# Optimization experiments

Measured on AMD Instinct MI355X. Metric: run time of the kernel, lower is better.

The kernel has to match this reference:

```python
import jax, jax.numpy as jnp
import numpy as np

B, Din, T, G = 8, 512, 1024, 128
DM, H, L, FF = 512, 8, 2, 2048
MAX_PERIOD = 10000.0


def _ln(x, s, b, eps=1e-5):
    m = x.mean(-1, keepdims=True)
    v = ((x - m) ** 2).mean(-1, keepdims=True)
    return (x - m) * jax.lax.rsqrt(v + eps) * s + b


def _rope(x, pos):
    # x: (B,H,S,Dh), pos: (S,)
    dh = x.shape[-1]
    half = dh // 2
    freqs = 1.0 / (MAX_PERIOD ** (jnp.arange(half, dtype=jnp.float32) / half))
    ang = pos[:, None] * freqs[None, :]              # (S, half)
    cos, sin = jnp.cos(ang), jnp.sin(ang)
    x1, x2 = x[..., :half], x[..., half:]
    return jnp.concatenate([x1 * cos - x2 * sin, x1 * sin + x2 * cos], axis=-1)


def _transformer(x, W_in, b_in, ln1_s, ln1_b, Wq, Wk, Wv, Wo, ls1,
                 ln2_s, ln2_b, W1, b1, W2, b2, ls2, lnf_s, lnf_b, W_out, b_out):
    # x: (B, Din, S) conv layout -> (B, S, DM)
    h = jnp.einsum('bds,de->bse', x, W_in) + b_in
    Bx, S, E = h.shape
    dh = E // H
    pos = jnp.arange(S, dtype=jnp.float32)
    scale = 1.0 / jnp.sqrt(jnp.asarray(dh, h.dtype))
    for l in range(Wq.shape[0]):
        y = _ln(h, ln1_s[l], ln1_b[l])
        q = (y @ Wq[l]).reshape(Bx, S, H, dh).transpose(0, 2, 1, 3)
        k = (y @ Wk[l]).reshape(Bx, S, H, dh).transpose(0, 2, 1, 3)
        v = (y @ Wv[l]).reshape(Bx, S, H, dh).transpose(0, 2, 1, 3)
        q, k = _rope(q, pos), _rope(k, pos)
        att = jax.nn.softmax(jnp.einsum('bhqd,bhkd->bhqk', q, k) * scale, axis=-1)
        o = jnp.einsum('bhqk,bhkd->bhqd', att, v).transpose(0, 2, 1, 3).reshape(Bx, S, E)
        h = h + ls1[l] * (o @ Wo[l])
        y = _ln(h, ln2_s[l], ln2_b[l])
        h = h + ls2[l] * (jax.nn.gelu(y @ W1[l] + b1[l]) @ W2[l] + b2[l])
    h = _ln(h, lnf_s, lnf_b)
    return (h @ W_out + b_out).transpose(0, 2, 1)  # (B, Din, S)


def _forward(features, alignment_matrix, num_segments_per_item, params):
    Bx, D, Tt = features.shape
    Gx = alignment_matrix.shape[1]
    ar_t = jnp.arange(Tt, dtype=jnp.int32)
    ar_g = jnp.arange(Gx, dtype=jnp.int32)
    group_mask = ar_g[None, :] < num_segments_per_item[:, None]          # (B,G)
    group_last = (alignment_matrix * ar_t.astype(features.dtype)).max(axis=2).astype(jnp.int32)  # (B,G)
    valid_last = jnp.where(group_mask, group_last, -1)
    frame_lengths = valid_last.max(axis=1) + 1                            # (B,)
    frame_mask = ar_t[None, :] < frame_lengths[:, None]                   # (B,T)
    last_for_count = jnp.where(group_mask, group_last, Tt + 1)
    num_q_before = jnp.sum(last_for_count[:, :, None] < ar_t[None, None, :], axis=1).astype(jnp.int32)  # (B,T)
    frame_dest = ar_t[None, :] + num_q_before                             # (B,T)
    query_dest = group_last + ar_g[None, :] + 1                           # (B,G)
    # mean-pooled query init
    summed = jnp.einsum('bgt,bdt->bgd', alignment_matrix, features)
    counts = jnp.maximum(alignment_matrix.sum(axis=2), 1.0)
    queries = (summed / counts[..., None]).transpose(0, 2, 1)             # (B,D,G)
    source_seq = jnp.concatenate([features, queries], axis=2)             # (B,D,T+G)
    dest = jnp.concatenate([frame_dest, query_dest], axis=1)              # (B,T+G)
    smask = jnp.concatenate([frame_mask, group_mask], axis=1)
    dest_m = jnp.where(smask, dest, Tt + Gx)
    perm = jnp.argsort(dest_m, axis=1)                                    # (B,T+G)
    interleaved = jnp.take_along_axis(source_seq, perm[:, None, :], axis=2)
    tout = _transformer(interleaved, *params)                             # (B,D,T+G)
    inv_perm = jnp.argsort(perm, axis=1)
    qpos = inv_perm[:, Tt:]                                               # (B,G)
    agg = jnp.take_along_axis(tout, qpos[:, None, :], axis=2)             # (B,D,G)
    return jnp.where(group_mask[:, None, :], agg, 0.0)


def setup_inputs() -> dict:
    key = jax.random.key(0)
    ks = jax.random.split(key, 8)
    rng = np.random.default_rng(0)
    align = np.zeros((B, G, T), np.float32)
    num_seg = np.zeros((B,), np.int32)
    for b in range(B):
        n = int(rng.integers(G // 2, G + 1))
        cuts = np.sort(rng.choice(np.arange(1, T), n - 1, replace=False))
        gid = np.searchsorted(cuts, np.arange(T), side='right')
        align[b, gid, np.arange(T)] = 1.0
        num_seg[b] = n
    s = 0.02
    return {
        'features': jax.random.normal(ks[0], (B, Din, T), jnp.float32),
        'alignment_matrix': jnp.asarray(align),
        'num_segments_per_item': jnp.asarray(num_seg),
        'W_in': jax.random.normal(ks[1], (Din, DM), jnp.float32) * s,
        'b_in': jnp.zeros((DM,), jnp.float32),
        'ln1_s': jnp.ones((L, DM), jnp.float32), 'ln1_b': jnp.zeros((L, DM), jnp.float32),
        'Wq': jax.random.normal(ks[2], (L, DM, DM), jnp.float32) * s,
        'Wk': jax.random.normal(ks[3], (L, DM, DM), jnp.float32) * s,
        'Wv': jax.random.normal(ks[4], (L, DM, DM), jnp.float32) * s,
        'Wo': jax.random.normal(ks[5], (L, DM, DM), jnp.float32) * s,
        'ls1': 0.01 * jnp.ones((L, DM), jnp.float32),
        'ln2_s': jnp.ones((L, DM), jnp.float32), 'ln2_b': jnp.zeros((L, DM), jnp.float32),
        'W1': jax.random.normal(ks[6], (L, DM, FF), jnp.float32) * s,
        'b1': jnp.zeros((L, FF), jnp.float32),
        'W2': jax.random.normal(ks[7], (L, FF, DM), jnp.float32) * s,
        'b2': jnp.zeros((L, DM), jnp.float32),
        'ls2': 0.01 * jnp.ones((L, DM), jnp.float32),
        'lnf_s': jnp.ones((DM,), jnp.float32), 'lnf_b': jnp.zeros((DM,), jnp.float32),
        'W_out': jax.random.normal(jax.random.fold_in(key, 9), (DM, Din), jnp.float32) * s,
        'b_out': jnp.zeros((Din,), jnp.float32),
    }


def reference(features, alignment_matrix, num_segments_per_item, W_in, b_in, ln1_s, ln1_b,
              Wq, Wk, Wv, Wo, ls1, ln2_s, ln2_b, W1, b1, W2, b2, ls2, lnf_s, lnf_b, W_out, b_out):
    params = (W_in, b_in, ln1_s, ln1_b, Wq, Wk, Wv, Wo, ls1,
              ln2_s, ln2_b, W1, b1, W2, b2, ls2, lnf_s, lnf_b, W_out, b_out)
    return _forward(features, alignment_matrix, num_segments_per_item, params)
```

## Files before the change

### kernel.cpp

```cpp
#include <hip/hip_runtime.h>
#include <hip/hip_bf16.h>
#include <math.h>

#define NB   8
#define NT   1024
#define NG   128
#define NS   1152
#define NDIN 512
#define NDM  512
#define NH   8
#define NDH  64
#define NFF  2048
#define NL   2

typedef __attribute__((ext_vector_type(4))) float  floatx4;
typedef __attribute__((ext_vector_type(8))) short  shortx8;

__device__ __forceinline__ float gelu_f(float x) {
    float u = 1.5957691216057308f * (x + 0.044715f * x * x * x);
    return x / (1.0f + __expf(-u));
}

__device__ __forceinline__ void gload_lds16(const void* g, void* l) {
    __builtin_amdgcn_global_load_lds((const __attribute__((address_space(1))) unsigned int*)g,
                                     (__attribute__((address_space(3))) unsigned int*)l, 16, 0, 0);
}

__device__ __forceinline__ short f2bfs(float x) {
    __hip_bfloat16 h = __float2bfloat16(x);
    return *(short*)&h;
}
__device__ __forceinline__ unsigned pack_bf2_rz(float a, float b) {
    unsigned au = *(unsigned*)&a, bu = *(unsigned*)&b;
    return (au >> 16) | (bu & 0xFFFF0000u);
}

__device__ __forceinline__ void wtile(const float* __restrict__ src,
        __hip_bfloat16* __restrict__ dst, int K, int N, int i, int tid, short tile[32][33])
{
    const int gx = N / 32;
    const int n0 = (i % gx) * 32;
    const int k0 = (i / gx) * 32;
    {
        const int r = tid >> 3, c4 = (tid & 7) * 4;
        float4 v = *(const float4*)&src[(size_t)(k0 + r) * N + n0 + c4];
        tile[c4 + 0][r] = f2bfs(v.x);
        tile[c4 + 1][r] = f2bfs(v.y);
        tile[c4 + 2][r] = f2bfs(v.z);
        tile[c4 + 3][r] = f2bfs(v.w);
    }
    __syncthreads();
    {
        const int r = tid >> 3, c4 = (tid & 7) * 4;
        short* dp = (short*)dst + (size_t)(n0 + r) * K + k0 + c4;
        short4 v;
        v.x = tile[r][c4 + 0]; v.y = tile[r][c4 + 1];
        v.z = tile[r][c4 + 2]; v.w = tile[r][c4 + 3];
        *(short4*)dp = v;
    }
}

__global__ __launch_bounds__(256) void prep0_k(
        float2* __restrict__ tab,
        const float* __restrict__ features, float* __restrict__ featT,
        const float* W_in, const float* Wq, const float* Wk, const float* Wv,
        const float* Wo, const float* W1, const float* W2, const float* W_out,
        __hip_bfloat16* w_inT, __hip_bfloat16* wqkvT0, __hip_bfloat16* wqkvT1,
        __hip_bfloat16* woT0, __hip_bfloat16* woT1,
        __hip_bfloat16* w1T0, __hip_bfloat16* w1T1,
        __hip_bfloat16* w2T0, __hip_bfloat16* w2T1, __hip_bfloat16* woutT)
{
    __shared__ __align__(16) char smem[32 * 33 * 4];
    const int tid = threadIdx.x;
    const int blk = blockIdx.x;
    if (blk < 144) {
        const int idx = blk * 256 + tid;
        const int s = idx >> 5, i = idx & 31;
        const float fr = __expf(-(float)i * 0.28782313662425576f);
        const float ang = (float)s * fr;
        tab[idx] = make_float2(cosf(ang), sinf(ang));
    } else if (blk < 144 + 4096) {
        float (*tile)[33] = (float(*)[33])smem;
        const int v = blk - 144;
        const int t0 = (v & 31) * 32;
        const int d0 = ((v >> 5) & 15) * 32;
        const int b  = v >> 9;
        const int r = tid >> 3, c4 = (tid & 7) * 4;
        {
            float4 w = *(const float4*)&features[((size_t)(b * NDIN + d0 + r)) * NT + t0 + c4];
            tile[c4 + 0][r] = w.x; tile[c4 + 1][r] = w.y;
            tile[c4 + 2][r] = w.z; tile[c4 + 3][r] = w.w;
        }
        __syncthreads();
        {
            float4 w;
            w.x = tile[r][c4 + 0]; w.y = tile[r][c4 + 1];
            w.z = tile[r][c4 + 2]; w.w = tile[r][c4 + 3];
            *(float4*)&featT[((size_t)(b * NT + t0 + r)) * NDIN + d0 + c4] = w;
        }
    } else {
        short (*tile)[33] = (short(*)[33])smem;
        const int i = blk - (144 + 4096);
        const float* src; __hip_bfloat16* dst; int K, N, ti;
        if (i < 256) { src = W_in; dst = w_inT; K = 512; N = 512; ti = i; }
        else if (i < 6400) {
            int r = i - 256;
            const int l = r / 3072; r -= l * 3072;
            const size_t o5 = (size_t)l * 262144, o2 = (size_t)l * 1048576;
            if (r < 256)       { src = Wq + o5; dst = (l ? wqkvT1 : wqkvT0);          K = 512;  N = 512;  ti = r; }
            else if (r < 512)  { src = Wk + o5; dst = (l ? wqkvT1 : wqkvT0) + 262144; K = 512;  N = 512;  ti = r - 256; }
            else if (r < 768)  { src = Wv + o5; dst = (l ? wqkvT1 : wqkvT0) + 524288; K = 512;  N = 512;  ti = r - 512; }
            else if (r < 1024) { src = Wo + o5; dst = (l ? woT1 : woT0);              K = 512;  N = 512;  ti = r - 768; }
            else if (r < 2048) { src = W1 + o2; dst = (l ? w1T1 : w1T0);              K = 512;  N = 2048; ti = r - 1024; }
            else               { src = W2 + o2; dst = (l ? w2T1 : w2T0);              K = 2048; N = 512;  ti = r - 2048; }
        }
        else { src = W_out; dst = woutT; K = 512; N = 512; ti = i - 6400; }
        wtile(src, dst, K, N, ti, tid, tile);
    }
}

__global__ __launch_bounds__(256) void pool_k(const float* __restrict__ align,
        const float* __restrict__ featT, int* __restrict__ glast,
        float* __restrict__ queries)
{
    __shared__ float redf[256];
    __shared__ int   redi[256];
    __shared__ float aw[NT];
    const int bg = blockIdx.x;
    const int b = bg >> 7;
    const int tid = threadIdx.x;
    const float* arow = align + (size_t)bg * NT;
    float cnt = 0.f, last = 0.f;
    int tmin = NT;
    for (int t = tid; t < NT; t += 256) {
        float a = arow[t];
        cnt += a;
        last = fmaxf(last, a * (float)t);
        if (a > 0.f) tmin = min(tmin, t);
    }
    redf[tid] = cnt; __syncthreads();
    for (int s = 128; s > 0; s >>= 1) { if (tid < s) redf[tid] += redf[tid + s]; __syncthreads(); }
    float c = redf[0]; __syncthreads();
    redf[tid] = last; __syncthreads();
    for (int s = 128; s > 0; s >>= 1) { if (tid < s) redf[tid] = fmaxf(redf[tid], redf[tid + s]); __syncthreads(); }
    float l = redf[0];
    redi[tid] = tmin; __syncthreads();
    for (int s = 128; s > 0; s >>= 1) { if (tid < s) redi[tid] = min(redi[tid], redi[tid + s]); __syncthreads(); }
    const int t0 = redi[0];
    const int t1 = (int)l;
    if (tid == 0) glast[bg] = t1;
    __syncthreads();
    for (int t = t0 + tid; t <= t1; t += 256) aw[t - t0] = arow[t];
    __syncthreads();
    const float invc = 1.0f / fmaxf(c, 1.0f);
    const float* fT = featT + (size_t)b * NT * NDIN;
    for (int d = tid; d < NDIN; d += 256) {
        float s = 0.f;
        for (int t = t0; t <= t1; ++t) s += aw[t - t0] * fT[(size_t)t * NDIN + d];
        queries[(size_t)bg * NDIN + d] = s * invc;
    }
}

__global__ __launch_bounds__(256) void rank_k(const int* __restrict__ glast,
        const int* __restrict__ nsegp, int* __restrict__ perm, int* __restrict__ qpos)
{
    __shared__ int dm[NS];
    __shared__ int gl[NG];
    const int b = blockIdx.y;
    const int tid = threadIdx.x;
    const int j = blockIdx.x * 256 + tid;
    if (tid < NG) gl[tid] = glast[b * NG + tid];
    const int ns = nsegp[b];
    __syncthreads();
    for (int jj = tid; jj < NS; jj += 256) {
        int d;
        if (jj < NT) {
            int t = jj, nq = 0, flen = 0;
            for (int g = 0; g < ns; ++g) {
                flen = max(flen, gl[g] + 1);
                nq += (gl[g] < t) ? 1 : 0;
            }
            d = (t < flen) ? (t + nq) : NS;
        } else {
            int g = jj - NT;
            d = (g < ns) ? (gl[g] + g + 1) : NS;
        }
        dm[jj] = d;
    }
    __syncthreads();
    if (j < NS) {
        const int my = dm[j];
        int r = 0;
        for (int t = 0; t < NS; ++t) {
            int v2 = dm[t];
            r += (v2 < my || (v2 == my && t < j)) ? 1 : 0;
        }
        perm[b * NS + r] = j;
        if (j >= NT) qpos[b * NG + (j - NT)] = r;
    }
}

__global__ __launch_bounds__(256) void buildx_k(const float* __restrict__ featT,
        const float* __restrict__ queries, const int* __restrict__ perm,
        __hip_bfloat16* __restrict__ X)
{
    const int idx = blockIdx.x * 256 + threadIdx.x;
    if (idx >= NB * NS * (NDIN / 4)) return;
    const int dq = idx & 127;
    const int p = (idx >> 7) % NS;
    const int b = idx / (NS * 128);
    const int j = perm[b * NS + p];
    const float4* src = (j < NT)
        ? (const float4*)&featT[((size_t)(b * NT + j)) * NDIN]
        : (const float4*)&queries[((size_t)(b * NG + (j - NT))) * NDIN];
    float4 v = src[dq];
    short4 o;
    o.x = f2bfs(v.x); o.y = f2bfs(v.y); o.z = f2bfs(v.z); o.w = f2bfs(v.w);
    *(short4*)((short*)X + ((size_t)(b * NS + p)) * NDIN + dq * 4) = o;
}

__global__ __launch_bounds__(256) void bgemmw1_k(const __hip_bfloat16* __restrict__ A,
        const __hip_bfloat16* __restrict__ Bt, __hip_bfloat16* __restrict__ Cout,
        const float* __restrict__ bias, int M, int N, int K)
{
    __shared__ __align__(16) short SM[4][128 * 32];
    short* As0 = SM[0]; short* As1 = SM[1];
    short* Bs0 = SM[2]; short* Bs1 = SM[3];
    const int tid = threadIdx.x;
    const int wave = tid >> 6, lane = tid & 63;
    const int quad = lane >> 4, l16 = lane & 15;
    const int wm = wave >> 1, wn = wave & 1;
    const size_t bm = (size_t)blockIdx.y * 128, bn = (size_t)blockIdx.x * 128;
    const int sw = (l16 >> 1) & 3;
    const short* Ag = (const short*)A;
    const short* Bg = (const short*)Bt;
    const int lrow = lane >> 2;
    const int lchunk = (lane & 3) ^ ((lane >> 3) & 3);

    floatx4 acc[4][4];
#pragma unroll
    for (int i = 0; i < 4; ++i)
#pragma unroll
        for (int j = 0; j < 4; ++j) acc[i][j] = (floatx4){0.f, 0.f, 0.f, 0.f};

    for (int k0 = 0; k0 < K; k0 += 64) {
        __syncthreads();
#pragma unroll
        for (int c = 0; c < 2; ++c) {
            const int r0 = (c * 4 + wave) * 16;
            const size_t ra = (bm + r0 + lrow) * (size_t)K + k0 + lchunk * 8;
            const size_t rb = (bn + r0 + lrow) * (size_t)K + k0 + lchunk * 8;
            gload_lds16(Ag + ra,      &As0[r0 * 32]);
            gload_lds16(Ag + ra + 32, &As1[r0 * 32]);
            gload_lds16(Bg + rb,      &Bs0[r0 * 32]);
            gload_lds16(Bg + rb + 32, &Bs1[r0 * 32]);
        }
        __syncthreads();
#pragma unroll
        for (int h = 0; h < 2; ++h) {
            const short* Asrc = h ? As1 : As0;
            const short* Bsrc = h ? Bs1 : Bs0;
            shortx8 af[4], bf[4];
#pragma unroll
            for (int t = 0; t < 4; ++t) {
                af[t] = *(const shortx8*)&Asrc[(wm * 64 + t * 16 + l16) * 32 + ((quad ^ sw) * 8)];
                bf[t] = *(const shortx8*)&Bsrc[(wn * 64 + t * 16 + l16) * 32 + ((quad ^ sw) * 8)];
            }
#pragma unroll
            for (int mt = 0; mt < 4; ++mt)
#pragma unroll
                for (int nt = 0; nt < 4; ++nt)
                    acc[mt][nt] = __builtin_amdgcn_mfma_f32_16x16x32_bf16(af[mt], bf[nt], acc[mt][nt], 0, 0, 0);
        }
    }
    __syncthreads();
    const size_t mbase = bm + wm * 64;
    const size_t nbase = bn + wn * 64;
    short* ep = &SM[wave][0];
#pragma unroll
    for (int nt = 0; nt < 4; ++nt) {
        const size_t n = nbase + nt * 16 + l16;
        const float bz = bias[n];
        const int col = nt * 16 + l16;
#pragma unroll
        for (int mt = 0; mt < 4; ++mt)
#pragma unroll
            for (int r = 0; r < 4; ++r) {
                const int rl = mt * 16 + quad * 4 + r;
                float e = gelu_f(acc[mt][nt][r] + bz);
                ep[rl * 64 + (((col >> 3) ^ (rl & 7)) * 8) + (col & 7)] = f2bfs(e);
            }
    }
    __asm__ __volatile__("" ::: "memory");
#pragma unroll
    for (int c2 = 0; c2 < 8; ++c2) {
        const int rl = c2 * 8 + (lane >> 3);
        const int cc = lane & 7;
        shortx8 v = *(const shortx8*)&ep[rl * 64 + ((cc ^ (rl & 7)) * 8)];
        *(shortx8*)((short*)Cout + (mbase + rl) * N + nbase + cc * 8) = v;
    }
}

__global__ __launch_bounds__(256) void bgemmqkv_k(const __hip_bfloat16* __restrict__ A,
        const __hip_bfloat16* __restrict__ Bt, __hip_bfloat16* __restrict__ qh,
        __hip_bfloat16* __restrict__ kh, __hip_bfloat16* __restrict__ vT,
        const float2* __restrict__ tab)
{
    __shared__ __align__(16) short SM[4][128 * 32];
    short* As0 = SM[0]; short* As1 = SM[1];
    short* Bs0 = SM[2]; short* Bs1 = SM[3];
    const int tid = threadIdx.x;
    const int wave = tid >> 6, lane = tid & 63;
    const int quad = lane >> 4, l16 = lane & 15;
    const int wm = wave >> 1, wn = wave & 1;
    const size_t bm = (size_t)blockIdx.y * 128, bn = (size_t)blockIdx.x * 128;
    const int sw = (l16 >> 1) & 3;
    const int K = 512;
    const short* Ag = (const short*)A;
    const short* Bg = (const short*)Bt;
    const int lrow = lane >> 2;
    const int lchunk = (lane & 3) ^ ((lane >> 3) & 3);

    floatx4 acc[4][4];
#pragma unroll
    for (int i = 0; i < 4; ++i)
#pragma unroll
        for (int j = 0; j < 4; ++j) acc[i][j] = (floatx4){0.f, 0.f, 0.f, 0.f};

    for (int k0 = 0; k0 < K; k0 += 64) {
        __syncthreads();
#pragma unroll
        for (int c = 0; c < 2; ++c) {
            const int r0 = (c * 4 + wave) * 16;
            const size_t ra = (bm + r0 + lrow) * (size_t)K + k0 + lchunk * 8;
            const size_t rb = (bn + r0 + lrow) * (size_t)K + k0 + lchunk * 8;
            gload_lds16(Ag + ra,      &As0[r0 * 32]);
            gload_lds16(Ag + ra + 32, &As1[r0 * 32]);
            gload_lds16(Bg + rb,      &Bs0[r0 * 32]);
            gload_lds16(Bg + rb + 32, &Bs1[r0 * 32]);
        }
        __syncthreads();
#pragma unroll
        for (int h = 0; h < 2; ++h) {
            const short* Asrc = h ? As1 : As0;
            const short* Bsrc = h ? Bs1 : Bs0;
            shortx8 af[4], bf[4];
#pragma unroll
            for (int t = 0; t < 4; ++t) {
                af[t] = *(const shortx8*)&Asrc[(wm * 64 + t * 16 + l16) * 32 + ((quad ^ sw) * 8)];
                bf[t] = *(const shortx8*)&Bsrc[(wn * 64 + t * 16 + l16) * 32 + ((quad ^ sw) * 8)];
            }
#pragma unroll
            for (int mt = 0; mt < 4; ++mt)
#pragma unroll
                for (int nt = 0; nt < 4; ++nt)
                    acc[mt][nt] = __builtin_amdgcn_mfma_f32_16x16x32_bf16(af[mt], bf[nt], acc[mt][nt], 0, 0, 0);
        }
    }
    __syncthreads();
    short* ep = &SM[wave][0];
    const int bidx = (int)(bm / NS);
    const int sbase = (int)(bm - (size_t)bidx * NS) + wm * 64;
    const int region = (int)(bn >> 9);
    if (region < 2) {
        const float qsc = region ? 1.0f : 0.18033688011112043f;
        const int h = (int)((((int)bn & 511) + wn * 64) >> 6);
#pragma unroll
        for (int nt = 0; nt < 2; ++nt) {
            const int d1 = nt * 16 + l16, d2 = d1 + 32;
            const float2* tp = tab + d1;
#pragma unroll
            for (int mt = 0; mt < 4; ++mt)
#pragma unroll
                for (int r = 0; r < 4; ++r) {
                    const int sl = mt * 16 + quad * 4 + r;
                    const int s = sbase + sl;
                    float x1 = acc[mt][nt][r], x2 = acc[mt][nt + 2][r];
                    float2 cs = tp[s * 32];
                    ep[sl * 64 + (((d1 >> 3) ^ (sl & 7)) * 8) + (d1 & 7)] = f2bfs(qsc * (x1 * cs.x - x2 * cs.y));
                    ep[sl * 64 + (((d2 >> 3) ^ (sl & 7)) * 8) + (d2 & 7)] = f2bfs(qsc * (x1 * cs.y + x2 * cs.x));
                }
        }
        __asm__ __volatile__("" ::: "memory");
        short* dst = (short*)(region ? kh : qh) + ((size_t)(bidx * NH + h)) * NS * NDH;
#pragma unroll
        for (int c2 = 0; c2 < 8; ++c2) {
            const int sl = c2 * 8 + (lane >> 3);
            const int cc = lane & 7;
            shortx8 v = *(const shortx8*)&ep[sl * 64 + ((cc ^ (sl & 7)) * 8)];
            *(shortx8*)(dst + (size_t)(sbase + sl) * NDH + cc * 8) = v;
        }
    } else {
        const int base = (int)(bn - 1024) + wn * 64;
        const int h = base >> 6;
#pragma unroll
        for (int nt = 0; nt < 4; ++nt) {
            const int dl = nt * 16 + l16;
#pragma unroll
            for (int mt = 0; mt < 4; ++mt)
#pragma unroll
                for (int r = 0; r < 4; ++r) {
                    const int sl = mt * 16 + quad * 4 + r;
                    ep[dl * 64 + (((sl >> 3) ^ (dl & 7)) * 8) + (sl & 7)] = f2bfs(acc[mt][nt][r]);
                }
        }
        __asm__ __volatile__("" ::: "memory");
        short* vp = (short*)vT + ((size_t)(bidx * NH + h)) * NDH * NS;
#pragma unroll
        for (int c2 = 0; c2 < 8; ++c2) {
            const int dl = c2 * 8 + (lane >> 3);
            const int cc = lane & 7;
            shortx8 v = *(const shortx8*)&ep[dl * 64 + ((cc ^ (dl & 7)) * 8)];
            *(shortx8*)(vp + (size_t)dl * NS + sbase + cc * 8) = v;
        }
    }
}

template <int EPI>
__global__ __launch_bounds__(256) void bgemm64_k(const __hip_bfloat16* __restrict__ A,
        const __hip_bfloat16* __restrict__ Bt, void* __restrict__ Cout,
        const float* __restrict__ bias, const float* __restrict__ ls,
        const float* __restrict__ res, const int* __restrict__ nsegp, int M, int N, int K)
{
    __shared__ __align__(16) short As0[64 * 32], As1[64 * 32];
    __shared__ __align__(16) short Bs0[128 * 32], Bs1[128 * 32];
    const int tid = threadIdx.x;
    const int wave = tid >> 6, lane = tid & 63;
    const int quad = lane >> 4, l16 = lane & 15;
    const int wm = wave >> 1, wn = wave & 1;
    const size_t bm = (size_t)blockIdx.y * 64, bn = (size_t)blockIdx.x * 128;
    const int sw = (l16 >> 1) & 3;
    const short* Ag = (const short*)A;
    const short* Bg = (const short*)Bt;
    const int lrow = lane >> 2;
    const int lchunk = (lane & 3) ^ ((lane >> 3) & 3);

    floatx4 acc[2][4];
#pragma unroll
    for (int i = 0; i < 2; ++i)
#pragma unroll
        for (int j = 0; j < 4; ++j) acc[i][j] = (floatx4){0.f, 0.f, 0.f, 0.f};

    for (int k0 = 0; k0 < K; k0 += 64) {
        __syncthreads();
        {
            const int rA = wave * 16;
            const size_t ra = (bm + rA + lrow) * (size_t)K + k0 + lchunk * 8;
            gload_lds16(Ag + ra,      &As0[rA * 32]);
            gload_lds16(Ag + ra + 32, &As1[rA * 32]);
            const int rB = wave * 32;
            const size_t rb0 = (bn + rB + lrow) * (size_t)K + k0 + lchunk * 8;
            const size_t rb1 = (bn + rB + 16 + lrow) * (size_t)K + k0 + lchunk * 8;
            gload_lds16(Bg + rb0,      &Bs0[rB * 32]);
            gload_lds16(Bg + rb1,      &Bs0[(rB + 16) * 32]);
            gload_lds16(Bg + rb0 + 32, &Bs1[rB * 32]);
            gload_lds16(Bg + rb1 + 32, &Bs1[(rB + 16) * 32]);
        }
        __syncthreads();
#pragma unroll
        for (int h = 0; h < 2; ++h) {
            const short* Asrc = h ? As1 : As0;
            const short* Bsrc = h ? Bs1 : Bs0;
            shortx8 af[2], bf[4];
#pragma unroll
            for (int t = 0; t < 2; ++t)
                af[t] = *(const shortx8*)&Asrc[(wm * 32 + t * 16 + l16) * 32 + ((quad ^ sw) * 8)];
#pragma unroll
            for (int t = 0; t < 4; ++t)
                bf[t] = *(const shortx8*)&Bsrc[(wn * 64 + t * 16 + l16) * 32 + ((quad ^ sw) * 8)];
#pragma unroll
            for (int mt = 0; mt < 2; ++mt)
#pragma unroll
                for (int nt = 0; nt < 4; ++nt)
                    acc[mt][nt] = __builtin_amdgcn_mfma_f32_16x16x32_bf16(af[mt], bf[nt], acc[mt][nt], 0, 0, 0);
        }
    }
    const size_t mbase = bm + wm * 32;
    const size_t nbase = bn + wn * 64;
#pragma unroll
    for (int nt = 0; nt < 4; ++nt) {
        const size_t n = nbase + nt * 16 + l16;
        const float bz = bias ? bias[n] : 0.f;
        const float lz = (EPI == 2) ? ls[n] : 0.f;
#pragma unroll
        for (int mt = 0; mt < 2; ++mt) {
#pragma unroll
            for (int r = 0; r < 4; ++r) {
                const size_t m = mbase + mt * 16 + quad * 4 + r;
                float e = acc[mt][nt][r] + bz;
                if (EPI == 4) {
                    const int b = (int)(m >> 7), g = (int)(m & 127);
                    float val = (g < nsegp[b]) ? e : 0.0f;
                    ((float*)Cout)[(size_t)b * (NDIN * NG) + n * NG + g] = val;
                } else {
                    const size_t off = m * N + n;
                    if (EPI == 2) e = res[off] + lz * e;
                    ((float*)Cout)[off] = e;
                }
            }
        }
    }
}

__global__ __launch_bounds__(256) void lnw_k(const float* __restrict__ in,
        __hip_bfloat16* __restrict__ out, const float* __restrict__ gam, const float* __restrict__ bet)
{
    const int r = blockIdx.x * 4 + (threadIdx.x >> 6);
    const int t = threadIdx.x & 63;
    const float4* xp = (const float4*)(in + (size_t)r * NDM);
    float4 a = xp[t * 2], b4 = xp[t * 2 + 1];
    float s = a.x + a.y + a.z + a.w + b4.x + b4.y + b4.z + b4.w;
#pragma unroll
    for (int o = 1; o < 64; o <<= 1) s += __shfl_xor(s, o);
    const float mean = s * (1.0f / NDM);
    float dx[8] = {a.x - mean, a.y - mean, a.z - mean, a.w - mean,
                   b4.x - mean, b4.y - mean, b4.z - mean, b4.w - mean};
    float v = 0.f;
#pragma unroll
    for (int i = 0; i < 8; ++i) v += dx[i] * dx[i];
#pragma unroll
    for (int o = 1; o < 64; o <<= 1) v += __shfl_xor(v, o);
    const float inv = rsqrtf(v * (1.0f / NDM) + 1e-5f);
    const float4* gp = (const float4*)gam;
    const float4* bp = (const float4*)bet;
    float4 g0 = gp[t * 2], g1 = gp[t * 2 + 1], q0 = bp[t * 2], q1 = bp[t * 2 + 1];
    shortx8 o8;
    o8[0] = f2bfs(dx[0] * inv * g0.x + q0.x);
    o8[1] = f2bfs(dx[1] * inv * g0.y + q0.y);
    o8[2] = f2bfs(dx[2] * inv * g0.z + q0.z);
    o8[3] = f2bfs(dx[3] * inv * g0.w + q0.w);
    o8[4] = f2bfs(dx[4] * inv * g1.x + q1.x);
    o8[5] = f2bfs(dx[5] * inv * g1.y + q1.y);
    o8[6] = f2bfs(dx[6] * inv * g1.z + q1.z);
    o8[7] = f2bfs(dx[7] * inv * g1.w + q1.w);
    *(shortx8*)((short*)out + (size_t)r * NDM + t * 8) = o8;
}

__global__ __launch_bounds__(64) void lnwg_k(const float* __restrict__ h,
        __hip_bfloat16* __restrict__ out, const float* __restrict__ gam, const float* __restrict__ bet,
        const int* __restrict__ qpos)
{
    const int r = blockIdx.x, t = threadIdx.x;
    const int b = r >> 7;
    const int src = qpos[r];
    const float4* xp = (const float4*)(h + ((size_t)(b * NS + src)) * NDM);
    float4 a = xp[t * 2], b4 = xp[t * 2 + 1];
    float s = a.x + a.y + a.z + a.w + b4.x + b4.y + b4.z + b4.w;
#pragma unroll
    for (int o = 1; o < 64; o <<= 1) s += __shfl_xor(s, o);
    const float mean = s * (1.0f / NDM);
    float dx[8] = {a.x - mean, a.y - mean, a.z - mean, a.w - mean,
                   b4.x - mean, b4.y - mean, b4.z - mean, b4.w - mean};
    float v = 0.f;
#pragma unroll
    for (int i = 0; i < 8; ++i) v += dx[i] * dx[i];
#pragma unroll
    for (int o = 1; o < 64; o <<= 1) v += __shfl_xor(v, o);
    const float inv = rsqrtf(v * (1.0f / NDM) + 1e-5f);
    const float4* gp = (const float4*)gam;
    const float4* bp = (const float4*)bet;
    float4 g0 = gp[t * 2], g1 = gp[t * 2 + 1], q0 = bp[t * 2], q1 = bp[t * 2 + 1];
    shortx8 o8;
    o8[0] = f2bfs(dx[0] * inv * g0.x + q0.x);
    o8[1] = f2bfs(dx[1] * inv * g0.y + q0.y);
    o8[2] = f2bfs(dx[2] * inv * g0.z + q0.z);
    o8[3] = f2bfs(dx[3] * inv * g0.w + q0.w);
    o8[4] = f2bfs(dx[4] * inv * g1.x + q1.x);
    o8[5] = f2bfs(dx[5] * inv * g1.y + q1.y);
    o8[6] = f2bfs(dx[6] * inv * g1.z + q1.z);
    o8[7] = f2bfs(dx[7] * inv * g1.w + q1.w);
    *(shortx8*)((short*)out + (size_t)r * NDM + t * 8) = o8;
}

#define FKT 64
#define FKP 68
#define NTL (NS / FKT)
__global__ __launch_bounds__(256) void fattn_k(const __hip_bfloat16* __restrict__ qb,
        const __hip_bfloat16* __restrict__ kb, const __hip_bfloat16* __restrict__ vbT,
        __hip_bfloat16* __restrict__ o)
{
    __shared__ __align__(16) short Ks[FKT * FKP];
    __shared__ __align__(16) short Vt[(NDH + 16) * FKP];
    __shared__ __align__(16) short Pl[64 * FKP];
    const int tid = threadIdx.x;
    const int wave = tid >> 6, lane = tid & 63;
    const int quad = lane >> 4, l16 = lane & 15;
    const int L = blockIdx.x;
    const int xcd = L & 7, sl = L >> 3;
    const int bh = (xcd << 3) | (sl & 7);
    const int q0 = (sl >> 3) * 64;
    const int bb = bh >> 3, hh = bh & 7;
    const short* qbase = (const short*)qb + (size_t)bh * NS * NDH;
    const short* kbase = (const short*)kb + (size_t)bh * NS * NDH;
    const short* vbase = (const short*)vbT + (size_t)bh * NDH * NS;

    shortx8 Qf0, Qf1;
    {
        const short* qp = qbase + (size_t)(q0 + wave * 16 + l16) * NDH + quad * 8;
        Qf0 = *(const shortx8*)qp;
        Qf1 = *(const shortx8*)(qp + 32);
    }
    {
        const int rr = 64 + (tid >> 4);
        const int cc = (tid & 15) * 4;
        short4 ones; ones.x = 0x3F80; ones.y = 0x3F80; ones.z = 0x3F80; ones.w = 0x3F80;
        *(short4*)&Vt[rr * FKP + cc] = ones;
    }
    __syncthreads();
    shortx8 Of0 = *(const shortx8*)&Vt[(64 + l16) * FKP + quad * 8];
    shortx8 Of1 = *(const shortx8*)&Vt[(64 + l16) * FKP + 32 + quad * 8];

    floatx4 Oacc[4];
#pragma unroll
    for (int i = 0; i < 4; ++i) Oacc[i] = (floatx4){0.f, 0.f, 0.f, 0.f};
    floatx4 Oacc5 = (floatx4){0.f, 0.f, 0.f, 0.f};

    const int sr = tid >> 2, sc = (tid & 3) * 16;
    const int prow = wave * 16 + l16;
    const short* kg = kbase + (size_t)sr * NDH + sc;
    const short* vg = vbase + (size_t)sr * NS + sc;
    shortx8 pk0 = *(const shortx8*)kg, pk1 = *(const shortx8*)(kg + 8);
    shortx8 pv0 = *(const shortx8*)vg, pv1 = *(const shortx8*)(vg + 8);

    for (int t = 0; t < NTL; ++t) {
        __syncthreads();
        *(shortx8*)&Ks[sr * FKP + sc]     = pk0;
        *(shortx8*)&Ks[sr * FKP + sc + 8] = pk1;
        *(shortx8*)&Vt[sr * FKP + sc]     = pv0;
        *(shortx8*)&Vt[sr * FKP + sc + 8] = pv1;
        __syncthreads();
        if (t + 1 < NTL) {
            kg += FKT * NDH; vg += FKT;
            pk0 = *(const shortx8*)kg; pk1 = *(const shortx8*)(kg + 8);
            pv0 = *(const shortx8*)vg; pv1 = *(const shortx8*)(vg + 8);
        }

        floatx4 S[4];
#pragma unroll
        for (int kbk = 0; kbk < 4; ++kbk) {
            shortx8 kf0 = *(const shortx8*)&Ks[(kbk * 16 + l16) * FKP + quad * 8];
            shortx8 kf1 = *(const shortx8*)&Ks[(kbk * 16 + l16) * FKP + 32 + quad * 8];
            floatx4 sa = (floatx4){0.f, 0.f, 0.f, 0.f};
            sa = __builtin_amdgcn_mfma_f32_16x16x32_bf16(kf0, Qf0, sa, 0, 0, 0);
            sa = __builtin_amdgcn_mfma_f32_16x16x32_bf16(kf1, Qf1, sa, 0, 0, 0);
            S[kbk] = sa;
        }
#pragma unroll
        for (int kbk = 0; kbk < 4; ++kbk) {
            uint2 u;
            u.x = pack_bf2_rz(exp2f(S[kbk][0]), exp2f(S[kbk][1]));
            u.y = pack_bf2_rz(exp2f(S[kbk][2]), exp2f(S[kbk][3]));
            *(uint2*)&Pl[prow * FKP + kbk * 16 + quad * 4] = u;
        }
        __asm__ __volatile__("" ::: "memory");
        shortx8 Pf0 = *(const shortx8*)&Pl[prow * FKP + quad * 8];
        shortx8 Pf1 = *(const shortx8*)&Pl[prow * FKP + 32 + quad * 8];
#pragma unroll
        for (int ct = 0; ct < 4; ++ct) {
            shortx8 vf0 = *(const shortx8*)&Vt[(ct * 16 + l16) * FKP + quad * 8];
            shortx8 vf1 = *(const shortx8*)&Vt[(ct * 16 + l16) * FKP + 32 + quad * 8];
            Oacc[ct] = __builtin_amdgcn_mfma_f32_16x16x32_bf16(Pf0, vf0, Oacc[ct], 0, 0, 0);
            Oacc[ct] = __builtin_amdgcn_mfma_f32_16x16x32_bf16(Pf1, vf1, Oacc[ct], 0, 0, 0);
        }
        Oacc5 = __builtin_amdgcn_mfma_f32_16x16x32_bf16(Pf0, Of0, Oacc5, 0, 0, 0);
        Oacc5 = __builtin_amdgcn_mfma_f32_16x16x32_bf16(Pf1, Of1, Oacc5, 0, 0, 0);
    }
    float lr[4];
#pragma unroll
    for (int i = 0; i < 4; ++i) lr[i] = __shfl(Oacc5[i], quad * 16);
#pragma unroll
    for (int i = 0; i < 4; ++i) {
        const float inv = 1.0f / lr[i];
        const int row = q0 + wave * 16 + quad * 4 + i;
        __hip_bfloat16* op = o + ((size_t)(bb * NS + row)) * NDM + hh * NDH + l16;
        op[0]  = __float2bfloat16(Oacc[0][i] * inv);
        op[16] = __float2bfloat16(Oacc[1][i] * inv);
        op[32] = __float2bfloat16(Oacc[2][i] * inv);
        op[48] = __float2bfloat16(Oacc[3][i] * inv);
    }
}

extern "C" void kernel_launch(void* const* d_in, const int* in_sizes, int n_in,
                              void* d_out, int out_size, void* d_ws, size_t ws_size,
                              hipStream_t stream) {
    const float* features = (const float*)d_in[0];
    const float* align    = (const float*)d_in[1];
    const int*   nseg     = (const int*)d_in[2];
    const float* W_in  = (const float*)d_in[3];
    const float* b_in  = (const float*)d_in[4];
    const float* ln1_s = (const float*)d_in[5];
    const float* ln1_b = (const float*)d_in[6];
    const float* Wq = (const float*)d_in[7];
    const float* Wk = (const float*)d_in[8];
    const float* Wv = (const float*)d_in[9];
    const float* Wo = (const float*)d_in[10];
    const float* ls1   = (const float*)d_in[11];
    const float* ln2_s = (const float*)d_in[12];
    const float* ln2_b = (const float*)d_in[13];
    const float* W1 = (const float*)d_in[14];
    const float* b1 = (const float*)d_in[15];
    const float* W2 = (const float*)d_in[16];
    const float* b2 = (const float*)d_in[17];
    const float* ls2   = (const float*)d_in[18];
    const float* lnf_s = (const float*)d_in[19];
    const float* lnf_b = (const float*)d_in[20];
    const float* W_out = (const float*)d_in[21];
    const float* b_out = (const float*)d_in[22];

    const size_t SZ_BSD = (size_t)NB * NS * NDM;

    float* p = (float*)d_ws;
    __hip_bfloat16* w_inT  = (__hip_bfloat16*)p;
    __hip_bfloat16* wqkvT0 = w_inT + 512 * 512;
    __hip_bfloat16* wqkvT1 = wqkvT0 + 1536 * 512;
    __hip_bfloat16* woT0   = wqkvT1 + 1536 * 512;
    __hip_bfloat16* woT1   = woT0 + 512 * 512;
    __hip_bfloat16* w1T0   = woT1 + 512 * 512;
    __hip_bfloat16* w1T1   = w1T0 + 2048 * 512;
    __hip_bfloat16* w2T0   = w1T1 + 2048 * 512;
    __hip_bfloat16* w2T1   = w2T0 + 512 * 2048;
    __hip_bfloat16* woutT  = w2T1 + 512 * 2048;
    int* glast = (int*)(woutT + 512 * 512);
    int* perm  = glast + NB * NG;
    int* qpos  = perm + NB * NS;
    float2* ropetab = (float2*)(qpos + NB * NG);
    p = (float*)(ropetab + NS * 32);

    float* featT = p; p += (size_t)NB * NT * NDIN;
    float* hbuf = p; p += SZ_BSD;
    __hip_bfloat16* ybuf = (__hip_bfloat16*)p;  p += SZ_BSD / 2;
    __hip_bfloat16* obuf = (__hip_bfloat16*)p;  p += SZ_BSD / 2;
    __hip_bfloat16* ubuf = (__hip_bfloat16*)p;  p += SZ_BSD * 2;
    __hip_bfloat16* xin  = (__hip_bfloat16*)p;  p += SZ_BSD / 2;
    float* quer = p; p += (size_t)NB * NG * NDIN;
    __hip_bfloat16* hq = (__hip_bfloat16*)p; p += (size_t)NB * NG * NDM / 2;
    const size_t needed = (size_t)((char*)p - (char*)d_ws);
    if (ws_size < needed) return;

    __hip_bfloat16* qh = ubuf;
    __hip_bfloat16* kh = ubuf + SZ_BSD;
    __hip_bfloat16* vT = xin;

    prep0_k<<<144 + 4096 + 6656, 256, 0, stream>>>(ropetab, features, featT,
            W_in, Wq, Wk, Wv, Wo, W1, W2, W_out,
            w_inT, wqkvT0, wqkvT1, woT0, woT1, w1T0, w1T1, w2T0, w2T1, woutT);
    pool_k<<<NB * NG, 256, 0, stream>>>(align, featT, glast, quer);
    rank_k<<<dim3((NS + 255) / 256, NB), 256, 0, stream>>>(glast, nseg, perm, qpos);
    buildx_k<<<(NB * NS * (NDIN / 4) + 255) / 256, 256, 0, stream>>>(featT, quer, perm, xin);

    const int M = NB * NS;
    bgemm64_k<0><<<dim3(NDM / 128, M / 64), 256, 0, stream>>>(xin, w_inT, hbuf, b_in, nullptr, nullptr, nullptr, M, NDM, NDIN);

    for (int l = 0; l < NL; ++l) {
        __hip_bfloat16* wqkvT = (l ? wqkvT1 : wqkvT0);
        __hip_bfloat16* woT   = (l ? woT1 : woT0);
        __hip_bfloat16* w1T   = (l ? w1T1 : w1T0);
        __hip_bfloat16* w2T   = (l ? w2T1 : w2T0);

        lnw_k<<<M / 4, 256, 0, stream>>>(hbuf, ybuf, ln1_s + l * NDM, ln1_b + l * NDM);
        bgemmqkv_k<<<dim3(1536 / 128, M / 128), 256, 0, stream>>>(ybuf, wqkvT, qh, kh, vT, ropetab);
        fattn_k<<<(NS / 64) * NH * NB, 256, 0, stream>>>(qh, kh, vT, obuf);
        bgemm64_k<2><<<dim3(NDM / 128, M / 64), 256, 0, stream>>>(obuf, woT, hbuf, nullptr, ls1 + l * NDM, hbuf, nullptr, M, NDM, NDM);
        lnw_k<<<M / 4, 256, 0, stream>>>(hbuf, ybuf, ln2_s + l * NDM, ln2_b + l * NDM);
        bgemmw1_k<<<dim3(NFF / 128, M / 128), 256, 0, stream>>>(ybuf, w1T, ubuf, b1 + l * NFF, M, NFF, NDM);
        bgemm64_k<2><<<dim3(NDM / 128, M / 64), 256, 0, stream>>>(ubuf, w2T, hbuf, b2 + l * NDM, ls2 + l * NDM, hbuf, nullptr, M, NDM, NFF);
    }

    lnwg_k<<<NB * NG, 64, 0, stream>>>(hbuf, hq, lnf_s, lnf_b, qpos);
    bgemm64_k<4><<<dim3(NDIN / 128, (NB * NG) / 64), 256, 0, stream>>>(hq, woutT, d_out, b_out, nullptr, nullptr, nseg, NB * NG, NDIN, NDM);
}
```

Baseline: 616.1 us.

## Software-pipeline QK^T one tile ahead with double-buffered V in flash attention

Restructures the attention loop so the QK^T scores for the next key tile are computed while the current tile's softmax and PV matmul run, with V double-buffered in LDS. It also raises wave priority around the MFMA blocks and replaces the LDS-loaded ones fragment with a register constant, which removes the shuffle for the row sum. This aims to hide LDS and exp latency behind MFMA work, at the cost of more registers (Sn) and more LDS, which may lower occupancy. Correctness relies on every lane's row-sum column of Oacc5 being identical now that all B entries are ones.

```diff
diff --git a/kernel.cpp b/kernel.cpp
--- a/kernel.cpp
+++ b/kernel.cpp
@@ -580,7 +580,7 @@
         __hip_bfloat16* __restrict__ o)
 {
     __shared__ __align__(16) short Ks[FKT * FKP];
-    __shared__ __align__(16) short Vt[(NDH + 16) * FKP];
+    __shared__ __align__(16) short Vt[2][NDH * FKP];
     __shared__ __align__(16) short Pl[64 * FKP];
     const int tid = threadIdx.x;
     const int wave = tid >> 6, lane = tid & 63;
@@ -600,15 +600,9 @@
         Qf0 = *(const shortx8*)qp;
         Qf1 = *(const shortx8*)(qp + 32);
     }
-    {
-        const int rr = 64 + (tid >> 4);
-        const int cc = (tid & 15) * 4;
-        short4 ones; ones.x = 0x3F80; ones.y = 0x3F80; ones.z = 0x3F80; ones.w = 0x3F80;
-        *(short4*)&Vt[rr * FKP + cc] = ones;
-    }
-    __syncthreads();
-    shortx8 Of0 = *(const shortx8*)&Vt[(64 + l16) * FKP + quad * 8];
-    shortx8 Of1 = *(const shortx8*)&Vt[(64 + l16) * FKP + 32 + quad * 8];
+    shortx8 Of;
+#pragma unroll
+    for (int i = 0; i < 8; ++i) Of[i] = 0x3F80;
 
     floatx4 Oacc[4];
 #pragma unroll
@@ -619,31 +613,59 @@
     const int prow = wave * 16 + l16;
     const short* kg = kbase + (size_t)sr * NDH + sc;
     const short* vg = vbase + (size_t)sr * NS + sc;
+
+    {
+        shortx8 a0 = *(const shortx8*)kg, a1 = *(const shortx8*)(kg + 8);
+        shortx8 b0 = *(const shortx8*)vg, b1 = *(const shortx8*)(vg + 8);
+        *(shortx8*)&Ks[sr * FKP + sc]        = a0;
+        *(shortx8*)&Ks[sr * FKP + sc + 8]    = a1;
+        *(shortx8*)&Vt[0][sr * FKP + sc]     = b0;
+        *(shortx8*)&Vt[0][sr * FKP + sc + 8] = b1;
+    }
+    kg += FKT * NDH; vg += FKT;
     shortx8 pk0 = *(const shortx8*)kg, pk1 = *(const shortx8*)(kg + 8);
     shortx8 pv0 = *(const shortx8*)vg, pv1 = *(const shortx8*)(vg + 8);
-
+    __syncthreads();
+
+    floatx4 S[4], Sn[4];
+#pragma unroll
+    for (int kbk = 0; kbk < 4; ++kbk) {
+        shortx8 kf0 = *(const shortx8*)&Ks[(kbk * 16 + l16) * FKP + quad * 8];
+        shortx8 kf1 = *(const shortx8*)&Ks[(kbk * 16 + l16) * FKP + 32 + quad * 8];
+        floatx4 sa = (floatx4){0.f, 0.f, 0.f, 0.f};
+        sa = __builtin_amdgcn_mfma_f32_16x16x32_bf16(kf0, Qf0, sa, 0, 0, 0);
+        sa = __builtin_amdgcn_mfma_f32_16x16x32_bf16(kf1, Qf1, sa, 0, 0, 0);
+        S[kbk] = sa;
+    }
+
+    int cur = 0;
+#pragma unroll 2
     for (int t = 0; t < NTL; ++t) {
         __syncthreads();
-        *(shortx8*)&Ks[sr * FKP + sc]     = pk0;
-        *(shortx8*)&Ks[sr * FKP + sc + 8] = pk1;
-        *(shortx8*)&Vt[sr * FKP + sc]     = pv0;
-        *(shortx8*)&Vt[sr * FKP + sc + 8] = pv1;
-        __syncthreads();
         if (t + 1 < NTL) {
-            kg += FKT * NDH; vg += FKT;
-            pk0 = *(const shortx8*)kg; pk1 = *(const shortx8*)(kg + 8);
-            pv0 = *(const shortx8*)vg; pv1 = *(const shortx8*)(vg + 8);
-        }
-
-        floatx4 S[4];
-#pragma unroll
-        for (int kbk = 0; kbk < 4; ++kbk) {
-            shortx8 kf0 = *(const shortx8*)&Ks[(kbk * 16 + l16) * FKP + quad * 8];
-            shortx8 kf1 = *(const shortx8*)&Ks[(kbk * 16 + l16) * FKP + 32 + quad * 8];
-            floatx4 sa = (floatx4){0.f, 0.f, 0.f, 0.f};
-            sa = __builtin_amdgcn_mfma_f32_16x16x32_bf16(kf0, Qf0, sa, 0, 0, 0);
-            sa = __builtin_amdgcn_mfma_f32_16x16x32_bf16(kf1, Qf1, sa, 0, 0, 0);
-            S[kbk] = sa;
+            *(shortx8*)&Ks[sr * FKP + sc]              = pk0;
+            *(shortx8*)&Ks[sr * FKP + sc + 8]          = pk1;
+            *(shortx8*)&Vt[cur ^ 1][sr * FKP + sc]     = pv0;
+            *(shortx8*)&Vt[cur ^ 1][sr * FKP + sc + 8] = pv1;
+        }
+        __syncthreads();
+        if (t + 1 < NTL) {
+            __builtin_amdgcn_s_setprio(1);
+#pragma unroll
+            for (int kbk = 0; kbk < 4; ++kbk) {
+                shortx8 kf0 = *(const shortx8*)&Ks[(kbk * 16 + l16) * FKP + quad * 8];
+                shortx8 kf1 = *(const shortx8*)&Ks[(kbk * 16 + l16) * FKP + 32 + quad * 8];
+                floatx4 sa = (floatx4){0.f, 0.f, 0.f, 0.f};
+                sa = __builtin_amdgcn_mfma_f32_16x16x32_bf16(kf0, Qf0, sa, 0, 0, 0);
+                sa = __builtin_amdgcn_mfma_f32_16x16x32_bf16(kf1, Qf1, sa, 0, 0, 0);
+                Sn[kbk] = sa;
+            }
+            __builtin_amdgcn_s_setprio(0);
+            if (t + 2 < NTL) {
+                kg += FKT * NDH; vg += FKT;
+                pk0 = *(const shortx8*)kg; pk1 = *(const shortx8*)(kg + 8);
+                pv0 = *(const shortx8*)vg; pv1 = *(const shortx8*)(vg + 8);
+            }
         }
 #pragma unroll
         for (int kbk = 0; kbk < 4; ++kbk) {
@@ -655,22 +677,24 @@
         __asm__ __volatile__("" ::: "memory");
         shortx8 Pf0 = *(const shortx8*)&Pl[prow * FKP + quad * 8];
         shortx8 Pf1 = *(const shortx8*)&Pl[prow * FKP + 32 + quad * 8];
+        __builtin_amdgcn_s_setprio(1);
 #pragma unroll
         for (int ct = 0; ct < 4; ++ct) {
-            shortx8 vf0 = *(const shortx8*)&Vt[(ct * 16 + l16) * FKP + quad * 8];
-            shortx8 vf1 = *(const shortx8*)&Vt[(ct * 16 + l16) * FKP + 32 + quad * 8];
+            shortx8 vf0 = *(const shortx8*)&Vt[cur][(ct * 16 + l16) * FKP + quad * 8];
+            shortx8 vf1 = *(const shortx8*)&Vt[cur][(ct * 16 + l16) * FKP + 32 + quad * 8];
             Oacc[ct] = __builtin_amdgcn_mfma_f32_16x16x32_bf16(Pf0, vf0, Oacc[ct], 0, 0, 0);
             Oacc[ct] = __builtin_amdgcn_mfma_f32_16x16x32_bf16(Pf1, vf1, Oacc[ct], 0, 0, 0);
         }
-        Oacc5 = __builtin_amdgcn_mfma_f32_16x16x32_bf16(Pf0, Of0, Oacc5, 0, 0, 0);
-        Oacc5 = __builtin_amdgcn_mfma_f32_16x16x32_bf16(Pf1, Of1, Oacc5, 0, 0, 0);
-    }
-    float lr[4];
-#pragma unroll
-    for (int i = 0; i < 4; ++i) lr[i] = __shfl(Oacc5[i], quad * 16);
+        Oacc5 = __builtin_amdgcn_mfma_f32_16x16x32_bf16(Pf0, Of, Oacc5, 0, 0, 0);
+        Oacc5 = __builtin_amdgcn_mfma_f32_16x16x32_bf16(Pf1, Of, Oacc5, 0, 0, 0);
+        __builtin_amdgcn_s_setprio(0);
+#pragma unroll
+        for (int i = 0; i < 4; ++i) S[i] = Sn[i];
+        cur ^= 1;
+    }
 #pragma unroll
     for (int i = 0; i < 4; ++i) {
-        const float inv = 1.0f / lr[i];
+        const float inv = 1.0f / Oacc5[i];
         const int row = q0 + wave * 16 + quad * 4 + i;
         __hip_bfloat16* op = o + ((size_t)(bb * NS + row)) * NDM + hh * NDH + l16;
         op[0]  = __float2bfloat16(Oacc[0][i] * inv);
```

New measurement: 618.5 us. About the same (+0.4%).

## Double-buffer GEMM k-loop so global-to-LDS loads overlap MFMA compute

Applied to the files above, without the earlier changes.

Reworks the main loop of the three bf16 GEMM kernels from a single-stage load-then-compute scheme with a 64-wide k step into a ping-pong double-buffered pipeline with a 32-wide k step. The loads for the next k slice are issued into the alternate LDS buffer before the MFMAs on the current slice, aiming to hide global load latency behind compute. In exchange each barrier covers half as much compute, so there are twice as many barriers per kernel. Whether the loads actually overlap depends on how the compiler places waitcnt instructions around the async LDS loads.

```diff
diff --git a/kernel.cpp b/kernel.cpp
--- a/kernel.cpp
+++ b/kernel.cpp
@@ -224,8 +224,6 @@
         const float* __restrict__ bias, int M, int N, int K)
 {
     __shared__ __align__(16) short SM[4][128 * 32];
-    short* As0 = SM[0]; short* As1 = SM[1];
-    short* Bs0 = SM[2]; short* Bs1 = SM[3];
     const int tid = threadIdx.x;
     const int wave = tid >> 6, lane = tid & 63;
     const int quad = lane >> 4, l16 = lane & 15;
@@ -236,6 +234,7 @@
     const short* Bg = (const short*)Bt;
     const int lrow = lane >> 2;
     const int lchunk = (lane & 3) ^ ((lane >> 3) & 3);
+    const int rS = wave * 32;
 
     floatx4 acc[4][4];
 #pragma unroll
@@ -243,37 +242,40 @@
 #pragma unroll
         for (int j = 0; j < 4; ++j) acc[i][j] = (floatx4){0.f, 0.f, 0.f, 0.f};
 
-    for (int k0 = 0; k0 < K; k0 += 64) {
+    {
+        const size_t ra = (bm + rS + lrow) * (size_t)K + lchunk * 8;
+        const size_t rb = (bn + rS + lrow) * (size_t)K + lchunk * 8;
+        gload_lds16(Ag + ra,                    &SM[0][rS * 32]);
+        gload_lds16(Ag + ra + 16 * (size_t)K,   &SM[0][(rS + 16) * 32]);
+        gload_lds16(Bg + rb,                    &SM[2][rS * 32]);
+        gload_lds16(Bg + rb + 16 * (size_t)K,   &SM[2][(rS + 16) * 32]);
+    }
+    __syncthreads();
+    int cur = 0;
+    for (int k0 = 0; k0 < K; k0 += 32) {
+        if (k0 + 32 < K) {
+            const int nx = cur ^ 1;
+            const size_t ra = (bm + rS + lrow) * (size_t)K + (k0 + 32) + lchunk * 8;
+            const size_t rb = (bn + rS + lrow) * (size_t)K + (k0 + 32) + lchunk * 8;
+            gload_lds16(Ag + ra,                  &SM[nx][rS * 32]);
+            gload_lds16(Ag + ra + 16 * (size_t)K, &SM[nx][(rS + 16) * 32]);
+            gload_lds16(Bg + rb,                  &SM[2 + nx][rS * 32]);
+            gload_lds16(Bg + rb + 16 * (size_t)K, &SM[2 + nx][(rS + 16) * 32]);
+        }
+        shortx8 af[4], bf[4];
+#pragma unroll
+        for (int t = 0; t < 4; ++t) {
+            af[t] = *(const shortx8*)&SM[cur][(wm * 64 + t * 16 + l16) * 32 + ((quad ^ sw) * 8)];
+            bf[t] = *(const shortx8*)&SM[2 + cur][(wn * 64 + t * 16 + l16) * 32 + ((quad ^ sw) * 8)];
+        }
+#pragma unroll
+        for (int mt = 0; mt < 4; ++mt)
+#pragma unroll
+            for (int nt = 0; nt < 4; ++nt)
+                acc[mt][nt] = __builtin_amdgcn_mfma_f32_16x16x32_bf16(af[mt], bf[nt], acc[mt][nt], 0, 0, 0);
         __syncthreads();
-#pragma unroll
-        for (int c = 0; c < 2; ++c) {
-            const int r0 = (c * 4 + wave) * 16;
-            const size_t ra = (bm + r0 + lrow) * (size_t)K + k0 + lchunk * 8;
-            const size_t rb = (bn + r0 + lrow) * (size_t)K + k0 + lchunk * 8;
-            gload_lds16(Ag + ra,      &As0[r0 * 32]);
-            gload_lds16(Ag + ra + 32, &As1[r0 * 32]);
-            gload_lds16(Bg + rb,      &Bs0[r0 * 32]);
-            gload_lds16(Bg + rb + 32, &Bs1[r0 * 32]);
-        }
-        __syncthreads();
-#pragma unroll
-        for (int h = 0; h < 2; ++h) {
-            const short* Asrc = h ? As1 : As0;
-            const short* Bsrc = h ? Bs1 : Bs0;
-            shortx8 af[4], bf[4];
-#pragma unroll
-            for (int t = 0; t < 4; ++t) {
-                af[t] = *(const shortx8*)&Asrc[(wm * 64 + t * 16 + l16) * 32 + ((quad ^ sw) * 8)];
-                bf[t] = *(const shortx8*)&Bsrc[(wn * 64 + t * 16 + l16) * 32 + ((quad ^ sw) * 8)];
-            }
-#pragma unroll
-            for (int mt = 0; mt < 4; ++mt)
-#pragma unroll
-                for (int nt = 0; nt < 4; ++nt)
-                    acc[mt][nt] = __builtin_amdgcn_mfma_f32_16x16x32_bf16(af[mt], bf[nt], acc[mt][nt], 0, 0, 0);
-        }
-    }
-    __syncthreads();
+        cur ^= 1;
+    }
     const size_t mbase = bm + wm * 64;
     const size_t nbase = bn + wn * 64;
     short* ep = &SM[wave][0];
@@ -307,8 +309,6 @@
         const float2* __restrict__ tab)
 {
     __shared__ __align__(16) short SM[4][128 * 32];
-    short* As0 = SM[0]; short* As1 = SM[1];
-    short* Bs0 = SM[2]; short* Bs1 = SM[3];
     const int tid = threadIdx.x;
     const int wave = tid >> 6, lane = tid & 63;
     const int quad = lane >> 4, l16 = lane & 15;
@@ -320,6 +320,7 @@
     const short* Bg = (const short*)Bt;
     const int lrow = lane >> 2;
     const int lchunk = (lane & 3) ^ ((lane >> 3) & 3);
+    const int rS = wave * 32;
 
     floatx4 acc[4][4];
 #pragma unroll
@@ -327,37 +328,40 @@
 #pragma unroll
         for (int j = 0; j < 4; ++j) acc[i][j] = (floatx4){0.f, 0.f, 0.f, 0.f};
 
-    for (int k0 = 0; k0 < K; k0 += 64) {
+    {
+        const size_t ra = (bm + rS + lrow) * (size_t)K + lchunk * 8;
+        const size_t rb = (bn + rS + lrow) * (size_t)K + lchunk * 8;
+        gload_lds16(Ag + ra,                  &SM[0][rS * 32]);
+        gload_lds16(Ag + ra + 16 * (size_t)K, &SM[0][(rS + 16) * 32]);
+        gload_lds16(Bg + rb,                  &SM[2][rS * 32]);
+        gload_lds16(Bg + rb + 16 * (size_t)K, &SM[2][(rS + 16) * 32]);
+    }
+    __syncthreads();
+    int cur = 0;
+    for (int k0 = 0; k0 < K; k0 += 32) {
+        if (k0 + 32 < K) {
+            const int nx = cur ^ 1;
+            const size_t ra = (bm + rS + lrow) * (size_t)K + (k0 + 32) + lchunk * 8;
+            const size_t rb = (bn + rS + lrow) * (size_t)K + (k0 + 32) + lchunk * 8;
+            gload_lds16(Ag + ra,                  &SM[nx][rS * 32]);
+            gload_lds16(Ag + ra + 16 * (size_t)K, &SM[nx][(rS + 16) * 32]);
+            gload_lds16(Bg + rb,                  &SM[2 + nx][rS * 32]);
+            gload_lds16(Bg + rb + 16 * (size_t)K, &SM[2 + nx][(rS + 16) * 32]);
+        }
+        shortx8 af[4], bf[4];
+#pragma unroll
+        for (int t = 0; t < 4; ++t) {
+            af[t] = *(const shortx8*)&SM[cur][(wm * 64 + t * 16 + l16) * 32 + ((quad ^ sw) * 8)];
+            bf[t] = *(const shortx8*)&SM[2 + cur][(wn * 64 + t * 16 + l16) * 32 + ((quad ^ sw) * 8)];
+        }
+#pragma unroll
+        for (int mt = 0; mt < 4; ++mt)
+#pragma unroll
+            for (int nt = 0; nt < 4; ++nt)
+                acc[mt][nt] = __builtin_amdgcn_mfma_f32_16x16x32_bf16(af[mt], bf[nt], acc[mt][nt], 0, 0, 0);
         __syncthreads();
-#pragma unroll
-        for (int c = 0; c < 2; ++c) {
-            const int r0 = (c * 4 + wave) * 16;
-            const size_t ra = (bm + r0 + lrow) * (size_t)K + k0 + lchunk * 8;
-            const size_t rb = (bn + r0 + lrow) * (size_t)K + k0 + lchunk * 8;
-            gload_lds16(Ag + ra,      &As0[r0 * 32]);
-            gload_lds16(Ag + ra + 32, &As1[r0 * 32]);
-            gload_lds16(Bg + rb,      &Bs0[r0 * 32]);
-            gload_lds16(Bg + rb + 32, &Bs1[r0 * 32]);
-        }
-        __syncthreads();
-#pragma unroll
-        for (int h = 0; h < 2; ++h) {
-            const short* Asrc = h ? As1 : As0;
-            const short* Bsrc = h ? Bs1 : Bs0;
-            shortx8 af[4], bf[4];
-#pragma unroll
-            for (int t = 0; t < 4; ++t) {
-                af[t] = *(const shortx8*)&Asrc[(wm * 64 + t * 16 + l16) * 32 + ((quad ^ sw) * 8)];
-                bf[t] = *(const shortx8*)&Bsrc[(wn * 64 + t * 16 + l16) * 32 + ((quad ^ sw) * 8)];
-            }
-#pragma unroll
-            for (int mt = 0; mt < 4; ++mt)
-#pragma unroll
-                for (int nt = 0; nt < 4; ++nt)
-                    acc[mt][nt] = __builtin_amdgcn_mfma_f32_16x16x32_bf16(af[mt], bf[nt], acc[mt][nt], 0, 0, 0);
-        }
-    }
-    __syncthreads();
+        cur ^= 1;
+    }
     short* ep = &SM[wave][0];
     const int bidx = (int)(bm / NS);
     const int sbase = (int)(bm - (size_t)bidx * NS) + wm * 64;
@@ -422,8 +426,8 @@
         const float* __restrict__ bias, const float* __restrict__ ls,
         const float* __restrict__ res, const int* __restrict__ nsegp, int M, int N, int K)
 {
-    __shared__ __align__(16) short As0[64 * 32], As1[64 * 32];
-    __shared__ __align__(16) short Bs0[128 * 32], Bs1[128 * 32];
+    __shared__ __align__(16) short As[2][64 * 32];
+    __shared__ __align__(16) short Bs[2][128 * 32];
     const int tid = threadIdx.x;
     const int wave = tid >> 6, lane = tid & 63;
     const int quad = lane >> 4, l16 = lane & 15;
@@ -434,6 +438,7 @@
     const short* Bg = (const short*)Bt;
     const int lrow = lane >> 2;
     const int lchunk = (lane & 3) ^ ((lane >> 3) & 3);
+    const int rA = wave * 16, rB = wave * 32;
 
     floatx4 acc[2][4];
 #pragma unroll
@@ -441,39 +446,38 @@
 #pragma unroll
         for (int j = 0; j < 4; ++j) acc[i][j] = (floatx4){0.f, 0.f, 0.f, 0.f};
 
-    for (int k0 = 0; k0 < K; k0 += 64) {
+    {
+        const size_t ra = (bm + rA + lrow) * (size_t)K + lchunk * 8;
+        const size_t rb = (bn + rB + lrow) * (size_t)K + lchunk * 8;
+        gload_lds16(Ag + ra,                  &As[0][rA * 32]);
+        gload_lds16(Bg + rb,                  &Bs[0][rB * 32]);
+        gload_lds16(Bg + rb + 16 * (size_t)K, &Bs[0][(rB + 16) * 32]);
+    }
+    __syncthreads();
+    int cur = 0;
+    for (int k0 = 0; k0 < K; k0 += 32) {
+        if (k0 + 32 < K) {
+            const int nx = cur ^ 1;
+            const size_t ra = (bm + rA + lrow) * (size_t)K + (k0 + 32) + lchunk * 8;
+            const size_t rb = (bn + rB + lrow) * (size_t)K + (k0 + 32) + lchunk * 8;
+            gload_lds16(Ag + ra,                  &As[nx][rA * 32]);
+            gload_lds16(Bg + rb,                  &Bs[nx][rB * 32]);
+            gload_lds16(Bg + rb + 16 * (size_t)K, &Bs[nx][(rB + 16) * 32]);
+        }
+        shortx8 af[2], bf[4];
+#pragma unroll
+        for (int t = 0; t < 2; ++t)
+            af[t] = *(const shortx8*)&As[cur][(wm * 32 + t * 16 + l16) * 32 + ((quad ^ sw) * 8)];
+#pragma unroll
+        for (int t = 0; t < 4; ++t)
+            bf[t] = *(const shortx8*)&Bs[cur][(wn * 64 + t * 16 + l16) * 32 + ((quad ^ sw) * 8)];
+#pragma unroll
+        for (int mt = 0; mt < 2; ++mt)
+#pragma unroll
+            for (int nt = 0; nt < 4; ++nt)
+                acc[mt][nt] = __builtin_amdgcn_mfma_f32_16x16x32_bf16(af[mt], bf[nt], acc[mt][nt], 0, 0, 0);
         __syncthreads();
-        {
-            const int rA = wave * 16;
-            const size_t ra = (bm + rA + lrow) * (size_t)K + k0 + lchunk * 8;
-            gload_lds16(Ag + ra,      &As0[rA * 32]);
-            gload_lds16(Ag + ra + 32, &As1[rA * 32]);
-            const int rB = wave * 32;
-            const size_t rb0 = (bn + rB + lrow) * (size_t)K + k0 + lchunk * 8;
-            const size_t rb1 = (bn + rB + 16 + lrow) * (size_t)K + k0 + lchunk * 8;
-            gload_lds16(Bg + rb0,      &Bs0[rB * 32]);
-            gload_lds16(Bg + rb1,      &Bs0[(rB + 16) * 32]);
-            gload_lds16(Bg + rb0 + 32, &Bs1[rB * 32]);
-            gload_lds16(Bg + rb1 + 32, &Bs1[(rB + 16) * 32]);
-        }
-        __syncthreads();
-#pragma unroll
-        for (int h = 0; h < 2; ++h) {
-            const short* Asrc = h ? As1 : As0;
-            const short* Bsrc = h ? Bs1 : Bs0;
-            shortx8 af[2], bf[4];
-#pragma unroll
-            for (int t = 0; t < 2; ++t)
-                af[t] = *(const shortx8*)&Asrc[(wm * 32 + t * 16 + l16) * 32 + ((quad ^ sw) * 8)];
-#pragma unroll
-            for (int t = 0; t < 4; ++t)
-                bf[t] = *(const shortx8*)&Bsrc[(wn * 64 + t * 16 + l16) * 32 + ((quad ^ sw) * 8)];
-#pragma unroll
-            for (int mt = 0; mt < 2; ++mt)
-#pragma unroll
-                for (int nt = 0; nt < 4; ++nt)
-                    acc[mt][nt] = __builtin_amdgcn_mfma_f32_16x16x32_bf16(af[mt], bf[nt], acc[mt][nt], 0, 0, 0);
-        }
+        cur ^= 1;
     }
     const size_t mbase = bm + wm * 32;
     const size_t nbase = bn + wn * 64;
```

Measured after the change: 613.1 us. No clear change (-0.5%).
